# Performance work log

Measured on AMD Instinct MI355X. Metric: run time of the kernel, lower is better.

The kernel has to match this reference:

```python
import jax, jax.numpy as jnp
import numpy as np

B, S, D, H = 4, 2048, 1024, 16
DH = D // H
FF = 4 * D
EPS = 1e-6

def _layer_norm(x, g, b):
    mu = jnp.mean(x, axis=-1, keepdims=True)
    var = jnp.mean((x - mu) ** 2, axis=-1, keepdims=True)
    return (x - mu) * jax.lax.rsqrt(var + EPS) * g + b

def setup_inputs() -> dict:
    key = jax.random.key(0)
    ks = jax.random.split(key, 12)
    sc = lambda fan_in: 1.0 / np.sqrt(fan_in)
    inp = {
        "x": jax.random.normal(ks[0], (B, S, D), jnp.float32),
        "mask": jnp.zeros((B, 1, 1, S), dtype=bool),
        "wq": jax.random.normal(ks[1], (D, D), jnp.float32) * sc(D),
        "bq": jnp.zeros((D,), jnp.float32),
        "wk": jax.random.normal(ks[2], (D, D), jnp.float32) * sc(D),
        "bk": jnp.zeros((D,), jnp.float32),
        "wv": jax.random.normal(ks[3], (D, D), jnp.float32) * sc(D),
        "bv": jnp.zeros((D,), jnp.float32),
        "wm": jax.random.normal(ks[4], (D, D), jnp.float32) * sc(D),
        "bm": jnp.zeros((D,), jnp.float32),
        "w1": jax.random.normal(ks[5], (D, FF), jnp.float32) * sc(D),
        "b1": jnp.zeros((FF,), jnp.float32),
        "w2": jax.random.normal(ks[6], (FF, D), jnp.float32) * sc(FF),
        "b2": jnp.zeros((D,), jnp.float32),
        "g1": jnp.ones((D,), jnp.float32),
        "be1": jnp.zeros((D,), jnp.float32),
        "g2": jnp.ones((D,), jnp.float32),
        "be2": jnp.zeros((D,), jnp.float32),
    }
    return inp

def reference(x, mask, wq, bq, wk, bk, wv, bv, wm, bm, w1, b1, w2, b2, g1, be1, g2, be2):
    # --- multi-head self-attention (eval mode: dropout = identity) ---
    q = (x @ wq + bq).reshape(B, S, H, DH).transpose(0, 2, 1, 3)  # [B,H,S,DH]
    k = (x @ wk + bk).reshape(B, S, H, DH).transpose(0, 2, 1, 3)
    v = (x @ wv + bv).reshape(B, S, H, DH).transpose(0, 2, 1, 3)
    scores = jnp.einsum("bhqd,bhkd->bhqk", q, k) / jnp.sqrt(jnp.float32(DH))
    scores = jnp.where(mask, jnp.float32(-1e9), scores)
    att = jax.nn.softmax(scores, axis=-1)
    ctx = jnp.einsum("bhqk,bhkd->bhqd", att, v)
    ctx = ctx.transpose(0, 2, 1, 3).reshape(B, S, D)
    atted = ctx @ wm + bm
    # --- residual + LN 1 ---
    x1 = _layer_norm(x + atted, g1, be1)
    # --- FFN: relu MLP (dropout identity in eval) ---
    h = jax.nn.relu(x1 @ w1 + b1)
    ff = h @ w2 + b2
    # --- residual + LN 2 ---
    return _layer_norm(x1 + ff, g2, be2)
```

## Files before the change

### kernel.cpp

```cpp
#include <hip/hip_runtime.h>

typedef unsigned short u16;
typedef __attribute__((ext_vector_type(8))) short short8;
typedef __attribute__((ext_vector_type(4))) float f32x4;

#define B_ 4
#define S_ 2048
#define D_ 1024
#define H_ 16
#define DH_ 64
#define FF_ 4096
#define M_ (B_ * S_)

#define QSCALE 0.18033688f

__device__ __forceinline__ u16 f2bf(float f) {
    union { float f; unsigned u; } v; v.f = f;
    unsigned r = v.u + 0x7FFFu + ((v.u >> 16) & 1u);
    return (u16)(r >> 16);
}
__device__ __forceinline__ u16 f2bf_fast(float f) {
    union { float f; unsigned u; } v; v.f = f;
    return (u16)((v.u + 0x8000u) >> 16);
}

__device__ __forceinline__ unsigned cvt_pk_bf16(float lo, float hi) {
    unsigned r;
    asm("v_cvt_pk_bf16_f32 %0, %1, %2" : "=v"(r) : "v"(lo), "v"(hi));
    return r;
}

__device__ __forceinline__ void gload16(const u16* g, u16* l) {
    __builtin_amdgcn_global_load_lds(
        (const __attribute__((address_space(1))) unsigned int*)g,
        (__attribute__((address_space(3))) unsigned int*)l, 16, 0, 0);
}

__global__ __launch_bounds__(256) void convert_f32_bf16(
    const float* __restrict__ in, u16* __restrict__ out, int n4)
{
    int idx = blockIdx.x * blockDim.x + threadIdx.x;
    int stride = gridDim.x * blockDim.x;
    for (int i = idx; i < n4; i += stride) {
        float4 v = ((const float4*)in)[i];
        uint2 o;
        o.x = (unsigned)f2bf(v.x) | ((unsigned)f2bf(v.y) << 16);
        o.y = (unsigned)f2bf(v.z) | ((unsigned)f2bf(v.w) << 16);
        ((uint2*)out)[i] = o;
    }
}

__global__ __launch_bounds__(256) void transpose_conv(
    const float* __restrict__ in, u16* __restrict__ out, int K, int N)
{
    __shared__ float t[32][33];
    int n0 = blockIdx.x * 32, k0 = blockIdx.y * 32;
    int tx = threadIdx.x, ty = threadIdx.y;
#pragma unroll
    for (int i = 0; i < 32; i += 8)
        t[ty + i][tx] = in[(size_t)(k0 + ty + i) * N + n0 + tx];
    __syncthreads();
#pragma unroll
    for (int i = 0; i < 32; i += 8)
        out[(size_t)(n0 + ty + i) * K + k0 + tx] = f2bf(t[tx][ty + i]);
}

__global__ __launch_bounds__(256) void concat_bias(
    const float* __restrict__ a, const float* __restrict__ b,
    const float* __restrict__ c, float* __restrict__ out)
{
    int i = blockIdx.x * 256 + threadIdx.x;
    float v = (i < 1024) ? a[i] : (i < 2048) ? b[i - 1024] : c[i - 2048];
    out[i] = v;
}

__global__ __launch_bounds__(256, 4) void gemm_bt(
    const u16* __restrict__ A, const u16* __restrict__ Bt,
    const float* __restrict__ bias, const float* __restrict__ res,
    float* __restrict__ outF, u16* __restrict__ outB,
    int M, int N, int K, int relu, int mode, int swz)
{
    __shared__ __align__(16) u16 As[128][64];
    __shared__ __align__(16) u16 Bs[128][64];

    int tid = threadIdx.x;
    int w = tid >> 6, lane = tid & 63, quad = lane >> 4, lm = lane & 15;
    int wr = w >> 1, wc = w & 1;

    int bx = blockIdx.x, by = blockIdx.y;
    if (swz) {
        int p = by * gridDim.x + bx;
        int c = p & 7, s = p >> 3;
        by = c * (gridDim.y >> 3) + s / gridDim.x;
        bx = s % gridDim.x;
    }
    int m0 = by * 128, n0 = bx * 128;

    f32x4 acc[4][4];
#pragma unroll
    for (int mt = 0; mt < 4; ++mt)
#pragma unroll
        for (int nt = 0; nt < 4; ++nt)
            acc[mt][nt] = (f32x4){0.f, 0.f, 0.f, 0.f};

    const u16* Ab = A + (size_t)m0 * K;
    const u16* Bb = Bt + (size_t)n0 * K;
    int srow = lane >> 3;
    int scolsw = ((lane & 7) ^ srow) * 8;
    int csw0 = ((0 * 4 + quad) ^ (lm & 7)) * 8;
    int csw1 = ((1 * 4 + quad) ^ (lm & 7)) * 8;

    for (int k0 = 0; k0 < K; k0 += 64) {
        __syncthreads();
#pragma unroll
        for (int i = 0; i < 4; ++i) {
            int r = w * 32 + i * 8;
            gload16(Ab + (size_t)(r + srow) * K + k0 + scolsw, &As[r][0]);
            gload16(Bb + (size_t)(r + srow) * K + k0 + scolsw, &Bs[r][0]);
        }
        __syncthreads();
#pragma unroll
        for (int kk = 0; kk < 2; ++kk) {
            int csw = kk ? csw1 : csw0;
            short8 af[4], bf[4];
#pragma unroll
            for (int mt = 0; mt < 4; ++mt)
                af[mt] = *(const short8*)&As[wr * 64 + mt * 16 + lm][csw];
#pragma unroll
            for (int nt = 0; nt < 4; ++nt)
                bf[nt] = *(const short8*)&Bs[wc * 64 + nt * 16 + lm][csw];
#pragma unroll
            for (int mt = 0; mt < 4; ++mt)
#pragma unroll
                for (int nt = 0; nt < 4; ++nt)
                    acc[mt][nt] = __builtin_amdgcn_mfma_f32_16x16x32_bf16(
                        af[mt], bf[nt], acc[mt][nt], 0, 0, 0);
        }
    }

#pragma unroll
    for (int mt = 0; mt < 4; ++mt)
#pragma unroll
        for (int nt = 0; nt < 4; ++nt)
#pragma unroll
            for (int r = 0; r < 4; ++r) {
                int row = m0 + wr * 64 + mt * 16 + quad * 4 + r;
                int col = n0 + wc * 64 + nt * 16 + lm;
                float v = acc[mt][nt][r] + bias[col];
                if (relu) v = fmaxf(v, 0.f);
                if (res) v += res[(size_t)row * N + col];
                if (outF) outF[(size_t)row * N + col] = v;
                if (outB) {
                    size_t oidx;
                    if (mode == 0) {
                        oidx = (size_t)row * N + col;
                    } else {
                        int part = col >> 10, c = col & 1023;
                        int b = row >> 11, s = row & 2047;
                        int h = c >> 6, dh = c & 63;
                        if (part == 0) v *= QSCALE;
                        size_t base = (size_t)part * ((size_t)M_ * D_);
                        if (part == 2)
                            oidx = base + (((size_t)(b * H_ + h)) * DH_ + dh) * S_ + s;
                        else
                            oidx = base + (((size_t)(b * H_ + h)) * S_ + s) * DH_ + dh;
                    }
                    outB[oidx] = f2bf(v);
                }
            }
}

__global__ __launch_bounds__(256, 3) void flash_attn(
    const u16* __restrict__ Q, const u16* __restrict__ K,
    const u16* __restrict__ Vt, const u16* __restrict__ ctxdummy, u16* __restrict__ ctx)
{
    __shared__ __align__(16) u16 Ks[2][64][64];
    __shared__ __align__(16) u16 Vs[2][64][64];
    __shared__ __align__(16) u16 Ps[128][68];

    int bh = blockIdx.x;
    int q0 = blockIdx.y * 128;
    int tid = threadIdx.x, w = tid >> 6, lane = tid & 63, quad = lane >> 4, lm = lane & 15;
    int srow = lane >> 3;
    int scolsw = ((lane & 7) ^ srow) * 8;
    int csw0 = (quad ^ (lm & 7)) * 8;
    int csw1 = ((4 + quad) ^ (lm & 7)) * 8;

    const u16* Qb = Q + ((size_t)bh * S_ + q0) * DH_;
    const u16* Kb = K + (size_t)bh * S_ * DH_;
    const u16* Vb = Vt + (size_t)bh * DH_ * S_;

#pragma unroll
    for (int i = 0; i < 2; ++i) {
        int r = w * 16 + i * 8;
        gload16(Kb + (size_t)(r + srow) * DH_ + scolsw, &Ks[0][r][0]);
        gload16(Vb + (size_t)(r + srow) * S_ + scolsw, &Vs[0][r][0]);
    }

    short8 qf[2][2];
#pragma unroll
    for (int mt = 0; mt < 2; ++mt)
#pragma unroll
        for (int kk = 0; kk < 2; ++kk)
            qf[mt][kk] = *(const short8*)(Qb + (size_t)(w * 32 + mt * 16 + lm) * DH_ +
                                          kk * 32 + quad * 8);

    float l_part[2] = {0.f, 0.f};
    f32x4 accO[2][4];
#pragma unroll
    for (int mt = 0; mt < 2; ++mt)
#pragma unroll
        for (int nt = 0; nt < 4; ++nt) accO[mt][nt] = (f32x4){0.f, 0.f, 0.f, 0.f};

    for (int kt = 0; kt < S_ / 64; ++kt) {
        int cur = kt & 1;
        __syncthreads();

        if (kt + 1 < S_ / 64) {
#pragma unroll
            for (int i = 0; i < 2; ++i) {
                int r = w * 16 + i * 8;
                gload16(Kb + ((size_t)((kt + 1) * 64 + r + srow)) * DH_ + scolsw,
                        &Ks[cur ^ 1][r][0]);
                gload16(Vb + (size_t)(r + srow) * S_ + (kt + 1) * 64 + scolsw,
                        &Vs[cur ^ 1][r][0]);
            }
        }

        f32x4 sc[2][4];
#pragma unroll
        for (int mt = 0; mt < 2; ++mt)
#pragma unroll
            for (int nt = 0; nt < 4; ++nt) sc[mt][nt] = (f32x4){0.f, 0.f, 0.f, 0.f};
        __builtin_amdgcn_s_setprio(1);
#pragma unroll
        for (int kk = 0; kk < 2; ++kk) {
            int csw = kk ? csw1 : csw0;
            short8 bk[4];
#pragma unroll
            for (int nt = 0; nt < 4; ++nt)
                bk[nt] = *(const short8*)&Ks[cur][nt * 16 + lm][csw];
#pragma unroll
            for (int mt = 0; mt < 2; ++mt)
#pragma unroll
                for (int nt = 0; nt < 4; ++nt)
                    sc[mt][nt] = __builtin_amdgcn_mfma_f32_16x16x32_bf16(
                        bk[nt], qf[mt][kk], sc[mt][nt], 0, 0, 0);
        }
        __builtin_amdgcn_s_setprio(0);

        short8 bv[2][4];
#pragma unroll
        for (int kk = 0; kk < 2; ++kk) {
            int csw = kk ? csw1 : csw0;
#pragma unroll
            for (int nt = 0; nt < 4; ++nt)
                bv[kk][nt] = *(const short8*)&Vs[cur][nt * 16 + lm][csw];
        }

#pragma unroll
        for (int mt = 0; mt < 2; ++mt) {
            float ls = 0.f;
            u16* prow = &Ps[w * 32 + mt * 16 + lm][0];
#pragma unroll
            for (int nt = 0; nt < 4; ++nt) {
                float p0 = __builtin_amdgcn_exp2f(sc[mt][nt][0]);
                float p1 = __builtin_amdgcn_exp2f(sc[mt][nt][1]);
                float p2 = __builtin_amdgcn_exp2f(sc[mt][nt][2]);
                float p3 = __builtin_amdgcn_exp2f(sc[mt][nt][3]);
                ls += (p0 + p1) + (p2 + p3);
                uint2 pw;
                pw.x = cvt_pk_bf16(p0, p1);
                pw.y = cvt_pk_bf16(p2, p3);
                *(uint2*)(prow + nt * 16 + quad * 4) = pw;
            }
            l_part[mt] += ls;
        }
        __builtin_amdgcn_sched_barrier(0);
        __builtin_amdgcn_s_waitcnt(0xC07F);
        __builtin_amdgcn_sched_barrier(0);

        __builtin_amdgcn_s_setprio(1);
#pragma unroll
        for (int kk = 0; kk < 2; ++kk) {
#pragma unroll
            for (int mt = 0; mt < 2; ++mt) {
                short8 a = *(const short8*)&Ps[w * 32 + mt * 16 + lm][kk * 32 + quad * 8];
#pragma unroll
                for (int nt = 0; nt < 4; ++nt)
                    accO[mt][nt] = __builtin_amdgcn_mfma_f32_16x16x32_bf16(
                        a, bv[kk][nt], accO[mt][nt], 0, 0, 0);
            }
        }
        __builtin_amdgcn_s_setprio(0);
    }

    int b = bh >> 4, h = bh & 15;
#pragma unroll
    for (int mt = 0; mt < 2; ++mt) {
        float l = l_part[mt];
        l += __shfl_xor(l, 16);
        l += __shfl_xor(l, 32);
        float inv = 1.0f / l;
#pragma unroll
        for (int r = 0; r < 4; ++r) {
            float invr = __shfl(inv, quad * 4 + r);
            int row = q0 + w * 32 + mt * 16 + quad * 4 + r;
#pragma unroll
            for (int nt = 0; nt < 4; ++nt)
                ctx[((size_t)(b * S_ + row)) * D_ + h * DH_ + nt * 16 + lm] =
                    f2bf(accO[mt][nt][r] * invr);
        }
    }
}

__global__ __launch_bounds__(256) void ln_kernel(
    const float* __restrict__ y, const float* __restrict__ g, const float* __restrict__ b,
    float* __restrict__ outF, u16* __restrict__ outB)
{
    int row = blockIdx.x;
    const float* yr = y + (size_t)row * D_;
    float v[4], s = 0.f, sq = 0.f;
#pragma unroll
    for (int i = 0; i < 4; ++i) {
        v[i] = yr[threadIdx.x + 256 * i];
        s += v[i]; sq += v[i] * v[i];
    }
#pragma unroll
    for (int off = 32; off; off >>= 1) { s += __shfl_down(s, off); sq += __shfl_down(sq, off); }
    __shared__ float rs[4], rq[4];
    int w = threadIdx.x >> 6, lane = threadIdx.x & 63;
    if (lane == 0) { rs[w] = s; rq[w] = sq; }
    __syncthreads();
    s = rs[0] + rs[1] + rs[2] + rs[3];
    sq = rq[0] + rq[1] + rq[2] + rq[3];
    float mu = s * (1.0f / D_);
    float var = sq * (1.0f / D_) - mu * mu;
    float rstd = rsqrtf(var + 1e-6f);
#pragma unroll
    for (int i = 0; i < 4; ++i) {
        int c = threadIdx.x + 256 * i;
        float o = (v[i] - mu) * rstd * g[c] + b[c];
        if (outF) outF[(size_t)row * D_ + c] = o;
        if (outB) outB[(size_t)row * D_ + c] = f2bf(o);
    }
}

extern "C" void kernel_launch(void* const* d_in, const int* in_sizes, int n_in,
                              void* d_out, int out_size, void* d_ws, size_t ws_size,
                              hipStream_t stream)
{
    const float* x  = (const float*)d_in[0];
    const float* wq = (const float*)d_in[2];  const float* bq = (const float*)d_in[3];
    const float* wk = (const float*)d_in[4];  const float* bk = (const float*)d_in[5];
    const float* wv = (const float*)d_in[6];  const float* bv = (const float*)d_in[7];
    const float* wm = (const float*)d_in[8];  const float* bm = (const float*)d_in[9];
    const float* w1 = (const float*)d_in[10]; const float* b1 = (const float*)d_in[11];
    const float* w2 = (const float*)d_in[12]; const float* b2 = (const float*)d_in[13];
    const float* g1 = (const float*)d_in[14]; const float* be1 = (const float*)d_in[15];
    const float* g2 = (const float*)d_in[16]; const float* be2 = (const float*)d_in[17];

    char* ws = (char*)d_ws;
    const size_t MB = 1024 * 1024;
    u16*   xb    = (u16*)(ws + 0 * MB);
    u16*   wqkvt = (u16*)(ws + 16 * MB);
    u16*   wmt   = (u16*)(ws + 22 * MB);
    u16*   w1t   = (u16*)(ws + 24 * MB);
    u16*   w2t   = (u16*)(ws + 32 * MB);
    u16*   Qh    = (u16*)(ws + 40 * MB);
    u16*   Kh    = (u16*)(ws + 56 * MB);
    u16*   Vth   = (u16*)(ws + 72 * MB);
    u16*   ctx   = (u16*)(ws + 88 * MB);
    float* bqkv  = (float*)(ws + 88 * MB);
    float* y1    = (float*)(ws + 40 * MB);
    float* x1f   = (float*)(ws + 104 * MB);
    u16*   x1b   = (u16*)(ws + 136 * MB);
    u16*   hb    = (u16*)(ws + 152 * MB);
    float* y2    = (float*)(ws + 40 * MB);

    dim3 tb(32, 8);

    convert_f32_bf16<<<2048, 256, 0, stream>>>(x, xb, (M_ * D_) / 4);
    transpose_conv<<<dim3(D_ / 32, D_ / 32), tb, 0, stream>>>(wq, wqkvt, D_, D_);
    transpose_conv<<<dim3(D_ / 32, D_ / 32), tb, 0, stream>>>(wk, wqkvt + (size_t)1024 * D_, D_, D_);
    transpose_conv<<<dim3(D_ / 32, D_ / 32), tb, 0, stream>>>(wv, wqkvt + (size_t)2048 * D_, D_, D_);
    transpose_conv<<<dim3(D_ / 32, D_ / 32), tb, 0, stream>>>(wm, wmt, D_, D_);
    transpose_conv<<<dim3(FF_ / 32, D_ / 32), tb, 0, stream>>>(w1, w1t, D_, FF_);
    transpose_conv<<<dim3(D_ / 32, FF_ / 32), tb, 0, stream>>>(w2, w2t, FF_, D_);
    concat_bias<<<12, 256, 0, stream>>>(bq, bk, bv, bqkv);

    gemm_bt<<<dim3(3 * D_ / 128, M_ / 128), 256, 0, stream>>>(
        xb, wqkvt, bqkv, nullptr, nullptr, Qh, M_, 3 * D_, D_, 0, 3, 0);

    flash_attn<<<dim3(B_ * H_, S_ / 128), 256, 0, stream>>>(Qh, Kh, Vth, nullptr, ctx);

    gemm_bt<<<dim3(D_ / 128, M_ / 128), 256, 0, stream>>>(
        ctx, wmt, bm, x, y1, nullptr, M_, D_, D_, 0, 0, 0);
    ln_kernel<<<M_, 256, 0, stream>>>(y1, g1, be1, x1f, x1b);

    gemm_bt<<<dim3(FF_ / 128, M_ / 128), 256, 0, stream>>>(
        x1b, w1t, b1, nullptr, nullptr, hb, M_, FF_, D_, 1, 0, 0);
    gemm_bt<<<dim3(D_ / 128, M_ / 128), 256, 0, stream>>>(
        hb, w2t, b2, x1f, y2, nullptr, M_, D_, FF_, 0, 0, 1);

    ln_kernel<<<M_, 256, 0, stream>>>(y2, g2, be2, (float*)d_out, nullptr);
}
```

Measured before the change: 589.8 us.

## Merge prep kernels into one launch and split-K the FFN down GEMM

The eight preprocessing kernels (x conversion, six weight transposes, bias concat) become a single launch, removing per-launch overhead and tail gaps. The FF2 GEMM (K=4096, only 512 tiles) is split into two K halves along grid z. Each half writes its partial sum to a separate fp32 buffer, and the second LayerNorm adds the two halves. The aim is more parallel blocks for that GEMM on a GPU with many CUs, at the cost of an extra fp32 partial buffer written and re-read.

Result: no change. 598.0 us (+1.4%).

```diff
diff --git a/kernel.cpp b/kernel.cpp
--- a/kernel.cpp
+++ b/kernel.cpp
@@ -19,10 +19,6 @@
     unsigned r = v.u + 0x7FFFu + ((v.u >> 16) & 1u);
     return (u16)(r >> 16);
 }
-__device__ __forceinline__ u16 f2bf_fast(float f) {
-    union { float f; unsigned u; } v; v.f = f;
-    return (u16)((v.u + 0x8000u) >> 16);
-}
 
 __device__ __forceinline__ unsigned cvt_pk_bf16(float lo, float hi) {
     unsigned r;
@@ -36,49 +32,69 @@
         (__attribute__((address_space(3))) unsigned int*)l, 16, 0, 0);
 }
 
-__global__ __launch_bounds__(256) void convert_f32_bf16(
-    const float* __restrict__ in, u16* __restrict__ out, int n4)
-{
-    int idx = blockIdx.x * blockDim.x + threadIdx.x;
-    int stride = gridDim.x * blockDim.x;
-    for (int i = idx; i < n4; i += stride) {
-        float4 v = ((const float4*)in)[i];
-        uint2 o;
-        o.x = (unsigned)f2bf(v.x) | ((unsigned)f2bf(v.y) << 16);
-        o.y = (unsigned)f2bf(v.z) | ((unsigned)f2bf(v.w) << 16);
-        ((uint2*)out)[i] = o;
-    }
-}
-
-__global__ __launch_bounds__(256) void transpose_conv(
-    const float* __restrict__ in, u16* __restrict__ out, int K, int N)
+__global__ __launch_bounds__(256) void prep_all(
+    const float* __restrict__ x, u16* __restrict__ xb,
+    const float* __restrict__ wq, const float* __restrict__ wk,
+    const float* __restrict__ wv, const float* __restrict__ wm,
+    const float* __restrict__ w1, const float* __restrict__ w2,
+    u16* __restrict__ wqkvt, u16* __restrict__ wmt,
+    u16* __restrict__ w1t, u16* __restrict__ w2t,
+    const float* __restrict__ bq, const float* __restrict__ bk,
+    const float* __restrict__ bv, float* __restrict__ bqkv)
 {
     __shared__ float t[32][33];
-    int n0 = blockIdx.x * 32, k0 = blockIdx.y * 32;
-    int tx = threadIdx.x, ty = threadIdx.y;
+    int id = blockIdx.x;
+
+    if (id < 2048) {
+        int n4 = (M_ * D_) / 4;
+        int idx = id * 256 + threadIdx.x;
+        for (int i = idx; i < n4; i += 2048 * 256) {
+            float4 v = ((const float4*)x)[i];
+            uint2 o;
+            o.x = (unsigned)f2bf(v.x) | ((unsigned)f2bf(v.y) << 16);
+            o.y = (unsigned)f2bf(v.z) | ((unsigned)f2bf(v.w) << 16);
+            ((uint2*)xb)[i] = o;
+        }
+        return;
+    }
+    id -= 2048;
+
+    const float* src; u16* dst; int K, N;
+    if (id < 4096) {
+        int which = id >> 10; id &= 1023;
+        K = D_; N = D_;
+        src = (which == 0) ? wq : (which == 1) ? wk : (which == 2) ? wv : wm;
+        dst = (which == 0) ? wqkvt
+            : (which == 1) ? (wqkvt + (size_t)1024 * D_)
+            : (which == 2) ? (wqkvt + (size_t)2048 * D_) : wmt;
+    } else if (id < 8192) {
+        id -= 4096; K = D_; N = FF_; src = w1; dst = w1t;
+    } else if (id < 12288) {
+        id -= 8192; K = FF_; N = D_; src = w2; dst = w2t;
+    } else {
+        int i = (id - 12288) * 256 + threadIdx.x;
+        float v = (i < 1024) ? bq[i] : (i < 2048) ? bk[i - 1024] : bv[i - 2048];
+        bqkv[i] = v;
+        return;
+    }
+
+    int nbx = N / 32;
+    int n0 = (id % nbx) * 32, k0 = (id / nbx) * 32;
+    int tx = threadIdx.x & 31, ty = threadIdx.x >> 5;
 #pragma unroll
     for (int i = 0; i < 32; i += 8)
-        t[ty + i][tx] = in[(size_t)(k0 + ty + i) * N + n0 + tx];
+        t[ty + i][tx] = src[(size_t)(k0 + ty + i) * N + n0 + tx];
     __syncthreads();
 #pragma unroll
     for (int i = 0; i < 32; i += 8)
-        out[(size_t)(n0 + ty + i) * K + k0 + tx] = f2bf(t[tx][ty + i]);
-}
-
-__global__ __launch_bounds__(256) void concat_bias(
-    const float* __restrict__ a, const float* __restrict__ b,
-    const float* __restrict__ c, float* __restrict__ out)
-{
-    int i = blockIdx.x * 256 + threadIdx.x;
-    float v = (i < 1024) ? a[i] : (i < 2048) ? b[i - 1024] : c[i - 2048];
-    out[i] = v;
+        dst[(size_t)(n0 + ty + i) * K + k0 + tx] = f2bf(t[tx][ty + i]);
 }
 
 __global__ __launch_bounds__(256, 4) void gemm_bt(
     const u16* __restrict__ A, const u16* __restrict__ Bt,
     const float* __restrict__ bias, const float* __restrict__ res,
-    float* __restrict__ outF, u16* __restrict__ outB,
-    int M, int N, int K, int relu, int mode, int swz)
+    float* __restrict__ outF, float* __restrict__ outF2, u16* __restrict__ outB,
+    int M, int N, int K, int relu, int mode, int swz, int kspl)
 {
     __shared__ __align__(16) u16 As[128][64];
     __shared__ __align__(16) u16 Bs[128][64];
@@ -95,6 +111,9 @@
         bx = s % gridDim.x;
     }
     int m0 = by * 128, n0 = bx * 128;
+    int kz = blockIdx.z;
+    int KS = K >> kspl;
+    int kbeg = kz * KS;
 
     f32x4 acc[4][4];
 #pragma unroll
@@ -110,7 +129,7 @@
     int csw0 = ((0 * 4 + quad) ^ (lm & 7)) * 8;
     int csw1 = ((1 * 4 + quad) ^ (lm & 7)) * 8;
 
-    for (int k0 = 0; k0 < K; k0 += 64) {
+    for (int k0 = kbeg; k0 < kbeg + KS; k0 += 64) {
         __syncthreads();
 #pragma unroll
         for (int i = 0; i < 4; ++i) {
@@ -138,6 +157,7 @@
         }
     }
 
+    float* oF = kz ? outF2 : outF;
 #pragma unroll
     for (int mt = 0; mt < 4; ++mt)
 #pragma unroll
@@ -146,10 +166,13 @@
             for (int r = 0; r < 4; ++r) {
                 int row = m0 + wr * 64 + mt * 16 + quad * 4 + r;
                 int col = n0 + wc * 64 + nt * 16 + lm;
-                float v = acc[mt][nt][r] + bias[col];
+                float v = acc[mt][nt][r];
+                if (!kz) {
+                    v += bias[col];
+                    if (res) v += res[(size_t)row * N + col];
+                }
                 if (relu) v = fmaxf(v, 0.f);
-                if (res) v += res[(size_t)row * N + col];
-                if (outF) outF[(size_t)row * N + col] = v;
+                if (oF) oF[(size_t)row * N + col] = v;
                 if (outB) {
                     size_t oidx;
                     if (mode == 0) {
@@ -315,15 +338,19 @@
 }
 
 __global__ __launch_bounds__(256) void ln_kernel(
-    const float* __restrict__ y, const float* __restrict__ g, const float* __restrict__ b,
+    const float* __restrict__ y, const float* __restrict__ yb,
+    const float* __restrict__ g, const float* __restrict__ b,
     float* __restrict__ outF, u16* __restrict__ outB)
 {
     int row = blockIdx.x;
     const float* yr = y + (size_t)row * D_;
+    const float* ybr = yb ? yb + (size_t)row * D_ : nullptr;
     float v[4], s = 0.f, sq = 0.f;
 #pragma unroll
     for (int i = 0; i < 4; ++i) {
-        v[i] = yr[threadIdx.x + 256 * i];
+        int c = threadIdx.x + 256 * i;
+        v[i] = yr[c];
+        if (ybr) v[i] += ybr[c];
         s += v[i]; sq += v[i] * v[i];
     }
 #pragma unroll
@@ -377,31 +404,24 @@
     u16*   x1b   = (u16*)(ws + 136 * MB);
     u16*   hb    = (u16*)(ws + 152 * MB);
     float* y2    = (float*)(ws + 40 * MB);
-
-    dim3 tb(32, 8);
-
-    convert_f32_bf16<<<2048, 256, 0, stream>>>(x, xb, (M_ * D_) / 4);
-    transpose_conv<<<dim3(D_ / 32, D_ / 32), tb, 0, stream>>>(wq, wqkvt, D_, D_);
-    transpose_conv<<<dim3(D_ / 32, D_ / 32), tb, 0, stream>>>(wk, wqkvt + (size_t)1024 * D_, D_, D_);
-    transpose_conv<<<dim3(D_ / 32, D_ / 32), tb, 0, stream>>>(wv, wqkvt + (size_t)2048 * D_, D_, D_);
-    transpose_conv<<<dim3(D_ / 32, D_ / 32), tb, 0, stream>>>(wm, wmt, D_, D_);
-    transpose_conv<<<dim3(FF_ / 32, D_ / 32), tb, 0, stream>>>(w1, w1t, D_, FF_);
-    transpose_conv<<<dim3(D_ / 32, FF_ / 32), tb, 0, stream>>>(w2, w2t, FF_, D_);
-    concat_bias<<<12, 256, 0, stream>>>(bq, bk, bv, bqkv);
+    float* y2b   = (float*)(ws + 72 * MB);
+
+    prep_all<<<14348, 256, 0, stream>>>(x, xb, wq, wk, wv, wm, w1, w2,
+                                        wqkvt, wmt, w1t, w2t, bq, bk, bv, bqkv);
 
     gemm_bt<<<dim3(3 * D_ / 128, M_ / 128), 256, 0, stream>>>(
-        xb, wqkvt, bqkv, nullptr, nullptr, Qh, M_, 3 * D_, D_, 0, 3, 0);
+        xb, wqkvt, bqkv, nullptr, nullptr, nullptr, Qh, M_, 3 * D_, D_, 0, 3, 0, 0);
 
     flash_attn<<<dim3(B_ * H_, S_ / 128), 256, 0, stream>>>(Qh, Kh, Vth, nullptr, ctx);
 
     gemm_bt<<<dim3(D_ / 128, M_ / 128), 256, 0, stream>>>(
-        ctx, wmt, bm, x, y1, nullptr, M_, D_, D_, 0, 0, 0);
-    ln_kernel<<<M_, 256, 0, stream>>>(y1, g1, be1, x1f, x1b);
+        ctx, wmt, bm, x, y1, nullptr, nullptr, M_, D_, D_, 0, 0, 0, 0);
+    ln_kernel<<<M_, 256, 0, stream>>>(y1, nullptr, g1, be1, x1f, x1b);
 
     gemm_bt<<<dim3(FF_ / 128, M_ / 128), 256, 0, stream>>>(
-        x1b, w1t, b1, nullptr, nullptr, hb, M_, FF_, D_, 1, 0, 0);
-    gemm_bt<<<dim3(D_ / 128, M_ / 128), 256, 0, stream>>>(
-        hb, w2t, b2, x1f, y2, nullptr, M_, D_, FF_, 0, 0, 1);
-
-    ln_kernel<<<M_, 256, 0, stream>>>(y2, g2, be2, (float*)d_out, nullptr);
-}
+        x1b, w1t, b1, nullptr, nullptr, nullptr, hb, M_, FF_, D_, 1, 0, 0, 0);
+    gemm_bt<<<dim3(D_ / 128, M_ / 128, 2), 256, 0, stream>>>(
+        hb, w2t, b2, x1f, y2, y2b, nullptr, M_, D_, FF_, 0, 0, 1, 1);
+
+    ln_kernel<<<M_, 256, 0, stream>>>(y2, y2b, g2, be2, (float*)d_out, nullptr);
+}
```
